# Kernel optimization log

Measured on AMD Instinct MI355X. Metric: run time of the kernel, lower is better.

## Reference

```python
import jax, jax.numpy as jnp
import numpy as np

D_MODEL = 1024
N_HEAD = 16
D_K = D_MODEL // N_HEAD


def setup_inputs() -> dict:
    key = jax.random.key(0)
    ks = jax.random.split(key, 11)
    B, T = 2, 2048
    s = 1.0 / np.sqrt(D_MODEL)
    return {
        "q": jax.random.normal(ks[0], (B, T, D_MODEL), jnp.float32),
        "k": jax.random.normal(ks[1], (B, T, D_MODEL), jnp.float32),
        "v": jax.random.normal(ks[2], (B, T, D_MODEL), jnp.float32),
        "w_q": jax.random.normal(ks[3], (D_MODEL, D_MODEL), jnp.float32) * s,
        "b_q": jax.random.normal(ks[4], (D_MODEL,), jnp.float32) * 0.01,
        "w_k": jax.random.normal(ks[5], (D_MODEL, D_MODEL), jnp.float32) * s,
        "b_k": jax.random.normal(ks[6], (D_MODEL,), jnp.float32) * 0.01,
        "w_v": jax.random.normal(ks[7], (D_MODEL, D_MODEL), jnp.float32) * s,
        "b_v": jax.random.normal(ks[8], (D_MODEL,), jnp.float32) * 0.01,
        "w_o": jax.random.normal(ks[9], (D_MODEL, D_MODEL), jnp.float32) * s,
        "b_o": jax.random.normal(ks[10], (D_MODEL,), jnp.float32) * 0.01,
    }


def reference(q, k, v, w_q, b_q, w_k, b_k, w_v, b_v, w_o, b_o):
    B, T, _ = q.shape
    # QKV projections -> [B, H, T, d_k]
    def proj(x, w, b):
        return (jnp.einsum('btd,de->bte', x, w) + b).reshape(B, T, N_HEAD, D_K).transpose(0, 2, 1, 3)
    qh = proj(q, w_q, b_q)
    kh = proj(k, w_k, b_k)
    vh = proj(v, w_v, b_v)
    scale = jnp.float32(1.0 / np.sqrt(D_K))
    scores = jnp.einsum('bhqd,bhkd->bhqk', qh, kh) * scale  # [B,H,T,T]
    attn = jax.nn.softmax(scores, axis=-1)
    # dropout is identity in eval mode
    out = jnp.einsum('bhqk,bhkd->bhqd', attn, vh)  # [B,H,T,d_k]
    out = out.transpose(0, 2, 1, 3).reshape(B, T, N_HEAD * D_K)
    return jnp.einsum('btd,de->bte', out, w_o) + b_o
```

## Files before the change

kernel.cpp:

```cpp
#include <hip/hip_runtime.h>
#include <stdint.h>

#define DEVI static __device__ __forceinline__

typedef float f32x4 __attribute__((ext_vector_type(4)));
typedef float f32x16 __attribute__((ext_vector_type(16)));
typedef short s16x8 __attribute__((ext_vector_type(8)));
typedef unsigned short u16x4 __attribute__((ext_vector_type(4)));
typedef uint32_t u32x2 __attribute__((ext_vector_type(2)));
typedef uint32_t u32x4 __attribute__((ext_vector_type(4)));

DEVI unsigned short f2bf(float f) {
  union { float f; uint32_t u; } v; v.f = f;
  uint32_t u = v.u;
  return (unsigned short)((u + 0x7fffu + ((u >> 16) & 1u)) >> 16);
}

DEVI float bf2f(unsigned short u) {
  union { uint32_t u; float f; } v;
  v.u = ((uint32_t)u) << 16;
  return v.f;
}

DEVI uint32_t cvtpk(float lo, float hi) {
  uint32_t r;
  asm("v_cvt_pk_bf16_f32 %0, %1, %2" : "=v"(r) : "v"(lo), "v"(hi));
  return r;
}

DEVI float fexp2(float x) {
#if __has_builtin(__builtin_amdgcn_exp2f)
  return __builtin_amdgcn_exp2f(x);
#else
  return exp2f(x);
#endif
}

DEVI float max3(float a, float b, float c) {
  float r;
  asm("v_max3_f32 %0, %1, %2, %3" : "=v"(r) : "v"(a), "v"(b), "v"(c));
  return r;
}

DEVI void pl32swap(uint32_t& a, uint32_t& b) {
#if __has_builtin(__builtin_amdgcn_permlane32_swap)
  u32x2 r = __builtin_amdgcn_permlane32_swap(a, b, false, false);
  a = r[0]; b = r[1];
#else
  asm("v_permlane32_swap_b32 %0, %1" : "+v"(a), "+v"(b));
#endif
}

DEVI float swap_half(float x, int hi) {
  uint32_t a = __float_as_uint(x), b = a;
  pl32swap(a, b);
  return hi ? __uint_as_float(a) : __uint_as_float(b);
}

DEVI void g2l16(const void* g, void* l) {
  __builtin_amdgcn_global_load_lds(
      (const __attribute__((address_space(1))) void*)g,
      (__attribute__((address_space(3))) void*)l, 16, 0, 0);
}

DEVI float vmax16(const f32x16& v) {
  float a = max3(v[0], v[1], v[2]);
  float b = max3(v[3], v[4], v[5]);
  float c = max3(v[6], v[7], v[8]);
  float d = max3(v[9], v[10], v[11]);
  float e = max3(v[12], v[13], v[14]);
  float x = max3(a, b, c);
  float y = max3(d, e, v[15]);
  return fmaxf(x, y);
}

DEVI float vsum16(const f32x16& v) {
  float a = (v[0] + v[1]) + (v[2] + v[3]);
  float b = (v[4] + v[5]) + (v[6] + v[7]);
  float c = (v[8] + v[9]) + (v[10] + v[11]);
  float d = (v[12] + v[13]) + (v[14] + v[15]);
  return (a + b) + (c + d);
}

DEVI void sm_group(f32x16& s0, f32x16& s1, float& m_run, float& l_run,
                   f32x16& o0, f32x16& o1, int hi, s16x8 (&pf)[4]) {
  float tm = fmaxf(vmax16(s0), vmax16(s1));
  tm = fmaxf(tm, swap_half(tm, hi));
  if (!__all(tm - m_run <= 8.0f)) {
    float mt = fmaxf(m_run, tm);
    float al = fexp2(m_run - mt);
    l_run *= al;
#pragma unroll
    for (int j = 0; j < 16; ++j) { o0[j] *= al; o1[j] *= al; }
    m_run = mt;
  }
#pragma unroll
  for (int j = 0; j < 16; ++j) s0[j] = fexp2(s0[j] - m_run);
#pragma unroll
  for (int j = 0; j < 16; ++j) s1[j] = fexp2(s1[j] - m_run);
  l_run += vsum16(s0) + vsum16(s1);
  {
    uint32_t w0 = cvtpk(s0[0], s0[1]), w1 = cvtpk(s0[2], s0[3]);
    uint32_t w2 = cvtpk(s0[4], s0[5]), w3 = cvtpk(s0[6], s0[7]);
    uint32_t w4 = cvtpk(s0[8], s0[9]), w5 = cvtpk(s0[10], s0[11]);
    uint32_t w6 = cvtpk(s0[12], s0[13]), w7 = cvtpk(s0[14], s0[15]);
    pl32swap(w0, w2); pl32swap(w1, w3); pl32swap(w4, w6); pl32swap(w5, w7);
    u32x4 f0 = {w0, w1, w2, w3}, f1 = {w4, w5, w6, w7};
    pf[0] = *(s16x8*)&f0;
    pf[1] = *(s16x8*)&f1;
  }
  {
    uint32_t w0 = cvtpk(s1[0], s1[1]), w1 = cvtpk(s1[2], s1[3]);
    uint32_t w2 = cvtpk(s1[4], s1[5]), w3 = cvtpk(s1[6], s1[7]);
    uint32_t w4 = cvtpk(s1[8], s1[9]), w5 = cvtpk(s1[10], s1[11]);
    uint32_t w6 = cvtpk(s1[12], s1[13]), w7 = cvtpk(s1[14], s1[15]);
    pl32swap(w0, w2); pl32swap(w1, w3); pl32swap(w4, w6); pl32swap(w5, w7);
    u32x4 f0 = {w0, w1, w2, w3}, f1 = {w4, w5, w6, w7};
    pf[2] = *(s16x8*)&f0;
    pf[3] = *(s16x8*)&f1;
  }
}

__global__ __launch_bounds__(256) void k_prep(
    const float* __restrict__ q, const float* __restrict__ k,
    const float* __restrict__ v, unsigned short* __restrict__ qkv,
    const float* __restrict__ w0, const float* __restrict__ w1,
    const float* __restrict__ w2, const float* __restrict__ w3,
    unsigned short* __restrict__ t0, unsigned short* __restrict__ t1,
    unsigned short* __restrict__ t2, unsigned short* __restrict__ t3) {
  __shared__ float tile[32][33];
  const int bx = blockIdx.x;
  if (bx < 3072) {
    const int y = bx >> 10;
    const float* in = y == 0 ? q : y == 1 ? k : v;
    unsigned short* o = qkv + (size_t)y * 4194304;
    int idx = (bx & 1023) * 256 + threadIdx.x;
    for (int i = idx * 4; i < 4194304; i += 1048576) {
      f32x4 x = *(const f32x4*)(in + i);
      u16x4 r;
      for (int j = 0; j < 4; ++j) r[j] = f2bf(x[j]);
      *(u16x4*)(o + i) = r;
    }
  } else {
    const int wb = bx - 3072;
    const int z = wb >> 10, tb = wb & 1023;
    const float* w = z == 0 ? w0 : z == 1 ? w1 : z == 2 ? w2 : w3;
    unsigned short* wt = z == 0 ? t0 : z == 1 ? t1 : z == 2 ? t2 : t3;
    const int n0 = (tb & 31) * 32, k0 = (tb >> 5) * 32;
    const int tx = threadIdx.x & 31, ty = threadIdx.x >> 5;
    for (int j = 0; j < 4; ++j)
      tile[ty + j * 8][tx] = w[(size_t)(k0 + ty + j * 8) * 1024 + n0 + tx];
    __syncthreads();
    for (int j = 0; j < 4; ++j)
      wt[(size_t)(n0 + ty + j * 8) * 1024 + k0 + tx] = f2bf(tile[tx][ty + j * 8]);
  }
}

__global__ __launch_bounds__(256) void k_gemm_multi(
    const unsigned short* A0, const unsigned short* A1, const unsigned short* A2,
    const unsigned short* B0, const unsigned short* B1, const unsigned short* B2,
    const float* c0, const float* c1, const float* c2,
    void* o0, void* o1, void* o2, int mode0) {
  constexpr int K = 1024;
  const int z = blockIdx.y;
  const unsigned short* A = z == 0 ? A0 : z == 1 ? A1 : A2;
  const unsigned short* Bt = z == 0 ? B0 : z == 1 ? B1 : B2;
  const float* bias = z == 0 ? c0 : z == 1 ? c1 : c2;
  void* outp = z == 0 ? o0 : z == 1 ? o1 : o2;
  const int MODE = mode0 + z;

  __shared__ __align__(16) unsigned short As[128 * 64];
  __shared__ __align__(16) unsigned short Bs[64 * 64];
  const int tid = threadIdx.x;
  const int lane = tid & 63, w = tid >> 6;
  const int g = lane >> 4, c = lane & 15;
  const int wgid = (blockIdx.x & 7) * 64 + (blockIdx.x >> 3);
  const int bm = wgid >> 4, bn = wgid & 15;
  const int m0 = bm * 128, n0 = bn * 64;
  const int wr = w >> 1, wc = w & 1;
  f32x4 acc[4][2] = {};

  for (int kt = 0; kt < 16; ++kt) {
    const int k0 = kt * 64;
    __syncthreads();
#pragma unroll
    for (int it = 0; it < 4; ++it) {
      int e = it * 256 + tid;
      int row = e >> 3, cwp = (e & 7) ^ (row & 7);
      g2l16(A + (size_t)(m0 + row) * K + k0 + cwp * 8,
            (char*)As + (it * 256 + (w << 6)) * 16);
    }
#pragma unroll
    for (int it = 0; it < 2; ++it) {
      int e = it * 256 + tid;
      int row = e >> 3, cwp = (e & 7) ^ (row & 7);
      g2l16(Bt + (size_t)(n0 + row) * K + k0 + cwp * 8,
            (char*)Bs + (it * 256 + (w << 6)) * 16);
    }
    __syncthreads();
    for (int kk = 0; kk < 2; ++kk) {
      s16x8 af[4], bfr[2];
      for (int mi = 0; mi < 4; ++mi) {
        int row = wr * 64 + mi * 16 + c;
        int ch = (kk * 4 + g) ^ (row & 7);
        af[mi] = *(const s16x8*)((const char*)As + row * 128 + ch * 16);
      }
      for (int ni = 0; ni < 2; ++ni) {
        int row = wc * 32 + ni * 16 + c;
        int ch = (kk * 4 + g) ^ (row & 7);
        bfr[ni] = *(const s16x8*)((const char*)Bs + row * 128 + ch * 16);
      }
      for (int mi = 0; mi < 4; ++mi)
        for (int ni = 0; ni < 2; ++ni)
          acc[mi][ni] = __builtin_amdgcn_mfma_f32_16x16x32_bf16(
              af[mi], bfr[ni], acc[mi][ni], 0, 0, 0);
    }
  }

  if (MODE == 0 || MODE == 1) {
    unsigned short* out = (unsigned short*)outp;
    const float scale = (MODE == 0) ? 0.1803368801111204f : 1.0f;
    for (int mi = 0; mi < 4; ++mi)
      for (int ni = 0; ni < 2; ++ni) {
        int row = m0 + wr * 64 + mi * 16 + g * 4;
        int col = n0 + wc * 32 + ni * 16 + c;
        float bb = bias[col];
        for (int r = 0; r < 4; ++r)
          out[(size_t)(row + r) * 1024 + col] = f2bf((acc[mi][ni][r] + bb) * scale);
      }
  } else if (MODE == 2) {
    unsigned short* vt = (unsigned short*)outp;
    const int bq = m0 >> 11, t0 = m0 & 2047;
    for (int mi = 0; mi < 4; ++mi)
      for (int ni = 0; ni < 2; ++ni) {
        int rowb = wr * 64 + mi * 16 + g * 4;
        int coll = wc * 32 + ni * 16 + c;
        float bb = bias[n0 + coll];
        u16x4 pk;
        for (int r = 0; r < 4; ++r) pk[r] = f2bf(acc[mi][ni][r] + bb);
        *(u16x4*)(vt + (size_t)(bq * 1024 + n0 + coll) * 2048 + t0 + rowb) = pk;
      }
  } else {
    float* out = (float*)outp;
    for (int mi = 0; mi < 4; ++mi)
      for (int ni = 0; ni < 2; ++ni) {
        int row = m0 + wr * 64 + mi * 16 + g * 4;
        int col = n0 + wc * 32 + ni * 16 + c;
        float bb = bias[col];
        for (int r = 0; r < 4; ++r)
          out[(size_t)(row + r) * 1024 + col] = acc[mi][ni][r] + bb;
      }
  }
}

__global__ __launch_bounds__(256) void k_attn(const unsigned short* __restrict__ Qp,
                                              const unsigned short* __restrict__ Kp,
                                              const unsigned short* __restrict__ Vt,
                                              unsigned short* __restrict__ Po0,
                                              unsigned short* __restrict__ Po1,
                                              float2* __restrict__ ml) {
  __shared__ __align__(16) unsigned short Ks[2][4096];
  __shared__ __align__(16) unsigned short Vs[3][4096];
  const int tid = threadIdx.x;
  const int lane = tid & 63, w = tid >> 6;
  const int l31 = lane & 31, hi = lane >> 5;
  const int blk = (blockIdx.x & 7) * 128 + (blockIdx.x >> 3);
  const int half = blk & 1, qt = (blk >> 1) & 15, bh = blk >> 5;
  const int b = bh >> 4, h = bh & 15;
  const int m0 = qt * 128 + w * 32;
  const size_t qkBase = (size_t)b * 2048 * 1024 + (size_t)h * 64;
  const size_t vtBase = ((size_t)b * 1024 + h * 64) * 2048;

  const unsigned short* qrow = Qp + qkBase + (size_t)(m0 + l31) * 1024;
  s16x8 bq[4];
#pragma unroll
  for (int s = 0; s < 4; ++s)
    bq[s] = *(const s16x8*)(qrow + s * 16 + hi * 8);

  const int srow = tid >> 2, c4 = tid & 3;
  const unsigned short* kg = Kp + qkBase + (size_t)srow * 1024 + c4 * 16 +
                             (size_t)half * 1048576;
  const unsigned short* vg = Vt + vtBase + (size_t)srow * 2048 + c4 * 16 +
                             half * 1024;
  int wof[2];
#pragma unroll
  for (int j = 0; j < 2; ++j)
    wof[j] = srow * 128 + (((c4 * 2 + j) ^ (srow & 7)) * 16);

  float m_run = -1e30f, l_run = 0.f;
  f32x16 o0 = {}, o1 = {};
  s16x8 pf[4];

  {
    s16x8 k0 = *(const s16x8*)(kg), k1 = *(const s16x8*)(kg + 8);
    s16x8 v0 = *(const s16x8*)(vg), v1 = *(const s16x8*)(vg + 8);
    *(s16x8*)((char*)&Ks[0][0] + wof[0]) = k0;
    *(s16x8*)((char*)&Ks[0][0] + wof[1]) = k1;
    *(s16x8*)((char*)&Vs[0][0] + wof[0]) = v0;
    *(s16x8*)((char*)&Vs[0][0] + wof[1]) = v1;
  }
  __syncthreads();

  const int rch = l31 & 7;
  int vr = 2, vw = 1;

#pragma unroll 1
  for (int t = 0; t < 16; ++t) {
    const int kcur = t & 1;
    s16x8 k0r, k1r, v0r, v1r;
    if (t < 15) {
      const unsigned short* kgt = kg + (size_t)(t + 1) * 65536;
      const unsigned short* vgt = vg + (t + 1) * 64;
      k0r = *(const s16x8*)(kgt); k1r = *(const s16x8*)(kgt + 8);
      v0r = *(const s16x8*)(vgt); v1r = *(const s16x8*)(vgt + 8);
    }
    const char* ks = (const char*)&Ks[kcur][0];

    f32x16 s0 = {}, s1 = {};
    __builtin_amdgcn_s_setprio(1);
#pragma unroll
    for (int ds = 0; ds < 4; ++ds) {
      int ch = (2 * ds + hi) ^ rch;
      s16x8 a0 = *(const s16x8*)(ks + l31 * 128 + ch * 16);
      s16x8 a1 = *(const s16x8*)(ks + (32 + l31) * 128 + ch * 16);
      s0 = __builtin_amdgcn_mfma_f32_32x32x16_bf16(a0, bq[ds], s0, 0, 0, 0);
      s1 = __builtin_amdgcn_mfma_f32_32x32x16_bf16(a1, bq[ds], s1, 0, 0, 0);
    }
    if (t > 0) {
      const char* vs = (const char*)&Vs[vr][0];
#pragma unroll
      for (int ksp = 0; ksp < 4; ++ksp) {
        int ch = (2 * ksp + hi) ^ rch;
        s16x8 a0 = *(const s16x8*)(vs + l31 * 128 + ch * 16);
        s16x8 a1 = *(const s16x8*)(vs + (32 + l31) * 128 + ch * 16);
        o0 = __builtin_amdgcn_mfma_f32_32x32x16_bf16(a0, pf[ksp], o0, 0, 0, 0);
        o1 = __builtin_amdgcn_mfma_f32_32x32x16_bf16(a1, pf[ksp], o1, 0, 0, 0);
      }
    }
    __builtin_amdgcn_s_setprio(0);

    sm_group(s0, s1, m_run, l_run, o0, o1, hi, pf);

    if (t < 15) {
      *(s16x8*)((char*)&Ks[kcur ^ 1][0] + wof[0]) = k0r;
      *(s16x8*)((char*)&Ks[kcur ^ 1][0] + wof[1]) = k1r;
      *(s16x8*)((char*)&Vs[vw][0] + wof[0]) = v0r;
      *(s16x8*)((char*)&Vs[vw][0] + wof[1]) = v1r;
    }
    __syncthreads();
    vr = vr == 2 ? 0 : vr + 1;
    vw = vw == 2 ? 0 : vw + 1;
  }

  {
    const char* vs = (const char*)&Vs[vr][0];
    __builtin_amdgcn_s_setprio(1);
#pragma unroll
    for (int ksp = 0; ksp < 4; ++ksp) {
      int ch = (2 * ksp + hi) ^ rch;
      s16x8 a0 = *(const s16x8*)(vs + l31 * 128 + ch * 16);
      s16x8 a1 = *(const s16x8*)(vs + (32 + l31) * 128 + ch * 16);
      o0 = __builtin_amdgcn_mfma_f32_32x32x16_bf16(a0, pf[ksp], o0, 0, 0, 0);
      o1 = __builtin_amdgcn_mfma_f32_32x32x16_bf16(a1, pf[ksp], o1, 0, 0, 0);
    }
    __builtin_amdgcn_s_setprio(0);
  }

  float lt = l_run + swap_half(l_run, hi);
  float inv = 1.0f / lt;
  unsigned short* Po = half ? Po1 : Po0;
  unsigned short* arow = Po + ((size_t)b * 2048 + m0 + l31) * 1024 + h * 64;
#pragma unroll
  for (int dblk = 0; dblk < 2; ++dblk) {
#pragma unroll
    for (int rq = 0; rq < 4; ++rq) {
      float e0 = (dblk ? o1[rq * 4 + 0] : o0[rq * 4 + 0]) * inv;
      float e1 = (dblk ? o1[rq * 4 + 1] : o0[rq * 4 + 1]) * inv;
      float e2 = (dblk ? o1[rq * 4 + 2] : o0[rq * 4 + 2]) * inv;
      float e3 = (dblk ? o1[rq * 4 + 3] : o0[rq * 4 + 3]) * inv;
      u32x2 pk;
      pk[0] = cvtpk(e0, e1);
      pk[1] = cvtpk(e2, e3);
      *(u32x2*)(arow + dblk * 32 + 8 * rq + 4 * hi) = pk;
    }
  }
  if (hi == 0) {
    int qid = ((b << 4) + h) * 2048 + m0 + l31;
    ml[half * 65536 + qid] = {m_run, lt};
  }
}

__global__ __launch_bounds__(256) void k_comb(const unsigned short* __restrict__ Po0,
                                              const unsigned short* __restrict__ Po1,
                                              const float2* __restrict__ ml,
                                              unsigned short* __restrict__ Att) {
  int idx = blockIdx.x * 256 + threadIdx.x;
  int base = idx * 8;
  int qrow = base >> 10, col = base & 1023;
  int h = col >> 6, b = qrow >> 11, t = qrow & 2047;
  int qid = ((b << 4) + h) * 2048 + t;
  float2 p0 = ml[qid], p1 = ml[65536 + qid];
  float ms = fmaxf(p0.x, p1.x);
  float a0 = fexp2(p0.x - ms) * p0.y, a1 = fexp2(p1.x - ms) * p1.y;
  float inv = 1.0f / (a0 + a1);
  float w0 = a0 * inv, w1 = a1 * inv;
  s16x8 v0 = *(const s16x8*)(Po0 + base);
  s16x8 v1 = *(const s16x8*)(Po1 + base);
  u32x4 pk;
#pragma unroll
  for (int j = 0; j < 4; ++j) {
    float e0 = w0 * bf2f((unsigned short)v0[2 * j]) + w1 * bf2f((unsigned short)v1[2 * j]);
    float e1 = w0 * bf2f((unsigned short)v0[2 * j + 1]) + w1 * bf2f((unsigned short)v1[2 * j + 1]);
    pk[j] = cvtpk(e0, e1);
  }
  *(u32x4*)(Att + base) = pk;
}

extern "C" void kernel_launch(void* const* d_in, const int* in_sizes, int n_in,
                              void* d_out, int out_size, void* d_ws, size_t ws_size,
                              hipStream_t stream) {
  const float* q = (const float*)d_in[0];
  const float* k = (const float*)d_in[1];
  const float* v = (const float*)d_in[2];
  const float* w_q = (const float*)d_in[3];
  const float* b_q = (const float*)d_in[4];
  const float* w_k = (const float*)d_in[5];
  const float* b_k = (const float*)d_in[6];
  const float* w_v = (const float*)d_in[7];
  const float* b_v = (const float*)d_in[8];
  const float* w_o = (const float*)d_in[9];
  const float* b_o = (const float*)d_in[10];

  unsigned short* s = (unsigned short*)d_ws;
  unsigned short* qbf = s;
  unsigned short* kbf = s + 4194304;
  unsigned short* vbf = s + 8388608;
  unsigned short* wqT = s + 12582912;
  unsigned short* wkT = s + 13631488;
  unsigned short* wvT = s + 14680064;
  unsigned short* woT = s + 15728640;
  unsigned short* Qp  = s + 16777216;
  unsigned short* Kp  = s + 20971520;
  unsigned short* Vt  = s + 25165824;
  unsigned short* Po0 = qbf;
  unsigned short* Po1 = kbf;
  unsigned short* Att = vbf;
  float2* ml = (float2*)wqT;

  k_prep<<<7168, 256, 0, stream>>>(q, k, v, qbf, w_q, w_k, w_v, w_o,
                                   wqT, wkT, wvT, woT);

  k_gemm_multi<<<dim3(512, 3), 256, 0, stream>>>(
      qbf, kbf, vbf, wqT, wkT, wvT, b_q, b_k, b_v,
      (void*)Qp, (void*)Kp, (void*)Vt, 0);

  k_attn<<<1024, 256, 0, stream>>>(Qp, Kp, Vt, Po0, Po1, ml);

  k_comb<<<2048, 256, 0, stream>>>(Po0, Po1, ml, Att);

  k_gemm_multi<<<dim3(512, 1), 256, 0, stream>>>(
      Att, Att, Att, woT, woT, woT, b_o, b_o, b_o,
      d_out, d_out, d_out, 3);
}
```

Measured before the change: 130.4 us.

## Load K/V tiles directly from global into registers, dropping LDS staging

The attention kernel no longer stages K and V tiles through shared memory with swizzled double/triple buffering and barriers. Each wave now loads its MFMA operands straight from global memory into registers, prefetching the next K tile and interleaving V loads with the QK and PV MFMAs. The PV product for each tile now runs in the same iteration as its softmax, rather than being deferred by one step. This removes LDS traffic and __syncthreads, but every wave redundantly fetches the same K/V data from global/L2 and register pressure rises.

```diff
diff --git a/kernel.cpp b/kernel.cpp
--- a/kernel.cpp
+++ b/kernel.cpp
@@ -259,8 +259,6 @@
                                               unsigned short* __restrict__ Po0,
                                               unsigned short* __restrict__ Po1,
                                               float2* __restrict__ ml) {
-  __shared__ __align__(16) unsigned short Ks[2][4096];
-  __shared__ __align__(16) unsigned short Vs[3][4096];
   const int tid = threadIdx.x;
   const int lane = tid & 63, w = tid >> 6;
   const int l31 = lane & 31, hi = lane >> 5;
@@ -277,92 +275,69 @@
   for (int s = 0; s < 4; ++s)
     bq[s] = *(const s16x8*)(qrow + s * 16 + hi * 8);
 
-  const int srow = tid >> 2, c4 = tid & 3;
-  const unsigned short* kg = Kp + qkBase + (size_t)srow * 1024 + c4 * 16 +
-                             (size_t)half * 1048576;
-  const unsigned short* vg = Vt + vtBase + (size_t)srow * 2048 + c4 * 16 +
-                             half * 1024;
-  int wof[2];
-#pragma unroll
-  for (int j = 0; j < 2; ++j)
-    wof[j] = srow * 128 + (((c4 * 2 + j) ^ (srow & 7)) * 16);
+  const unsigned short* kr0 = Kp + qkBase + (size_t)half * 1048576 +
+                              (size_t)l31 * 1024 + hi * 8;
+  const unsigned short* kr1 = kr0 + 32 * 1024;
+  const unsigned short* vr0 = Vt + vtBase + (size_t)l31 * 2048 + half * 1024 + hi * 8;
+  const unsigned short* vr1 = vr0 + 32 * 2048;
 
   float m_run = -1e30f, l_run = 0.f;
   f32x16 o0 = {}, o1 = {};
-  s16x8 pf[4];
-
-  {
-    s16x8 k0 = *(const s16x8*)(kg), k1 = *(const s16x8*)(kg + 8);
-    s16x8 v0 = *(const s16x8*)(vg), v1 = *(const s16x8*)(vg + 8);
-    *(s16x8*)((char*)&Ks[0][0] + wof[0]) = k0;
-    *(s16x8*)((char*)&Ks[0][0] + wof[1]) = k1;
-    *(s16x8*)((char*)&Vs[0][0] + wof[0]) = v0;
-    *(s16x8*)((char*)&Vs[0][0] + wof[1]) = v1;
-  }
-  __syncthreads();
-
-  const int rch = l31 & 7;
-  int vr = 2, vw = 1;
+  s16x8 ka[4], kb[4], va[4], vb[4], pf[4];
+
+#pragma unroll
+  for (int ds = 0; ds < 4; ++ds) {
+    ka[ds] = *(const s16x8*)(kr0 + ds * 16);
+    kb[ds] = *(const s16x8*)(kr1 + ds * 16);
+  }
 
 #pragma unroll 1
   for (int t = 0; t < 16; ++t) {
-    const int kcur = t & 1;
-    s16x8 k0r, k1r, v0r, v1r;
-    if (t < 15) {
-      const unsigned short* kgt = kg + (size_t)(t + 1) * 65536;
-      const unsigned short* vgt = vg + (t + 1) * 64;
-      k0r = *(const s16x8*)(kgt); k1r = *(const s16x8*)(kgt + 8);
-      v0r = *(const s16x8*)(vgt); v1r = *(const s16x8*)(vgt + 8);
-    }
-    const char* ks = (const char*)&Ks[kcur][0];
+    const unsigned short* vt0 = vr0 + t * 64;
+#pragma unroll
+    for (int ks = 0; ks < 4; ++ks) va[ks] = *(const s16x8*)(vt0 + ks * 16);
 
     f32x16 s0 = {}, s1 = {};
     __builtin_amdgcn_s_setprio(1);
 #pragma unroll
-    for (int ds = 0; ds < 4; ++ds) {
-      int ch = (2 * ds + hi) ^ rch;
-      s16x8 a0 = *(const s16x8*)(ks + l31 * 128 + ch * 16);
-      s16x8 a1 = *(const s16x8*)(ks + (32 + l31) * 128 + ch * 16);
-      s0 = __builtin_amdgcn_mfma_f32_32x32x16_bf16(a0, bq[ds], s0, 0, 0, 0);
-      s1 = __builtin_amdgcn_mfma_f32_32x32x16_bf16(a1, bq[ds], s1, 0, 0, 0);
-    }
-    if (t > 0) {
-      const char* vs = (const char*)&Vs[vr][0];
-#pragma unroll
-      for (int ksp = 0; ksp < 4; ++ksp) {
-        int ch = (2 * ksp + hi) ^ rch;
-        s16x8 a0 = *(const s16x8*)(vs + l31 * 128 + ch * 16);
-        s16x8 a1 = *(const s16x8*)(vs + (32 + l31) * 128 + ch * 16);
-        o0 = __builtin_amdgcn_mfma_f32_32x32x16_bf16(a0, pf[ksp], o0, 0, 0, 0);
-        o1 = __builtin_amdgcn_mfma_f32_32x32x16_bf16(a1, pf[ksp], o1, 0, 0, 0);
-      }
-    }
+    for (int ds = 0; ds < 4; ++ds)
+      s0 = __builtin_amdgcn_mfma_f32_32x32x16_bf16(ka[ds], bq[ds], s0, 0, 0, 0);
     __builtin_amdgcn_s_setprio(0);
 
+    const unsigned short* vt1 = vr1 + t * 64;
+#pragma unroll
+    for (int ks = 0; ks < 4; ++ks) vb[ks] = *(const s16x8*)(vt1 + ks * 16);
+
+    __builtin_amdgcn_s_setprio(1);
+#pragma unroll
+    for (int ds = 0; ds < 4; ++ds)
+      s1 = __builtin_amdgcn_mfma_f32_32x32x16_bf16(kb[ds], bq[ds], s1, 0, 0, 0);
+    __builtin_amdgcn_s_setprio(0);
+
+    if (t < 15) {
+      const unsigned short* kn0 = kr0 + (size_t)(t + 1) * 65536;
+#pragma unroll
+      for (int ds = 0; ds < 4; ++ds) ka[ds] = *(const s16x8*)(kn0 + ds * 16);
+    }
+
     sm_group(s0, s1, m_run, l_run, o0, o1, hi, pf);
 
+    __builtin_amdgcn_s_setprio(1);
+#pragma unroll
+    for (int ks = 0; ks < 4; ++ks)
+      o0 = __builtin_amdgcn_mfma_f32_32x32x16_bf16(va[ks], pf[ks], o0, 0, 0, 0);
+    __builtin_amdgcn_s_setprio(0);
+
     if (t < 15) {
-      *(s16x8*)((char*)&Ks[kcur ^ 1][0] + wof[0]) = k0r;
-      *(s16x8*)((char*)&Ks[kcur ^ 1][0] + wof[1]) = k1r;
-      *(s16x8*)((char*)&Vs[vw][0] + wof[0]) = v0r;
-      *(s16x8*)((char*)&Vs[vw][0] + wof[1]) = v1r;
-    }
-    __syncthreads();
-    vr = vr == 2 ? 0 : vr + 1;
-    vw = vw == 2 ? 0 : vw + 1;
-  }
-
-  {
-    const char* vs = (const char*)&Vs[vr][0];
+      const unsigned short* kn1 = kr1 + (size_t)(t + 1) * 65536;
+#pragma unroll
+      for (int ds = 0; ds < 4; ++ds) kb[ds] = *(const s16x8*)(kn1 + ds * 16);
+    }
+
     __builtin_amdgcn_s_setprio(1);
 #pragma unroll
-    for (int ksp = 0; ksp < 4; ++ksp) {
-      int ch = (2 * ksp + hi) ^ rch;
-      s16x8 a0 = *(const s16x8*)(vs + l31 * 128 + ch * 16);
-      s16x8 a1 = *(const s16x8*)(vs + (32 + l31) * 128 + ch * 16);
-      o0 = __builtin_amdgcn_mfma_f32_32x32x16_bf16(a0, pf[ksp], o0, 0, 0, 0);
-      o1 = __builtin_amdgcn_mfma_f32_32x32x16_bf16(a1, pf[ksp], o1, 0, 0, 0);
-    }
+    for (int ks = 0; ks < 4; ++ks)
+      o1 = __builtin_amdgcn_mfma_f32_32x32x16_bf16(vb[ks], pf[ks], o1, 0, 0, 0);
     __builtin_amdgcn_s_setprio(0);
   }
 
```

Result: slower. 192.7 us (+47.8%).
